# Performance work log

Hardware: AMD Instinct MI355X
Metric: run time of the kernel (lower is better)

## Reference

```python
import jax, jax.numpy as jnp
import numpy as np
import math

B = 2
D = 256
NH, NL, NP = 8, 4, 4
DH = D // NH
DFF = 1024
NLAYERS = 6
SHAPES = [(96, 96), (48, 48), (24, 24), (12, 12)]
CINS = [256, 512, 768, 1024]
LQ = sum(h * w for h, w in SHAPES)


def setup_inputs() -> dict:
    key = jax.random.key(0)
    ks = iter(jax.random.split(key, 64))
    inp = {}
    for i, (cin, (h, w)) in enumerate(zip(CINS, SHAPES)):
        inp[f"x{i+1}"] = jax.random.normal(next(ks), (B, cin, h, w), jnp.float32)
        inp[f"fc{i+1}_w"] = jax.random.normal(next(ks), (D, cin), jnp.float32) / np.sqrt(cin)
        inp[f"fc{i+1}_b"] = jnp.zeros((D,), jnp.float32)
    inp["gn_g"] = jnp.ones((4, D), jnp.float32)
    inp["gn_b"] = jnp.zeros((4, D), jnp.float32)
    inp["level_embed"] = jax.random.normal(next(ks), (4, D), jnp.float32)
    def lin(k, o, i_, s=1.0):
        return jax.random.normal(k, (NLAYERS, o, i_), jnp.float32) * (s / np.sqrt(i_))
    inp["off_w"] = lin(next(ks), NH * NL * NP * 2, D, 0.01)  # small, like zero-init offsets
    inp["off_b"] = jax.random.normal(next(ks), (NLAYERS, NH * NL * NP * 2), jnp.float32) * 0.5
    inp["aw_w"] = lin(next(ks), NH * NL * NP, D)
    inp["aw_b"] = jnp.zeros((NLAYERS, NH * NL * NP), jnp.float32)
    inp["val_w"] = lin(next(ks), D, D)
    inp["val_b"] = jnp.zeros((NLAYERS, D), jnp.float32)
    inp["out_w"] = lin(next(ks), D, D)
    inp["out_b"] = jnp.zeros((NLAYERS, D), jnp.float32)
    inp["ln1_g"] = jnp.ones((NLAYERS, D), jnp.float32)
    inp["ln1_b"] = jnp.zeros((NLAYERS, D), jnp.float32)
    inp["l1_w"] = lin(next(ks), DFF, D)
    inp["l1_b"] = jnp.zeros((NLAYERS, DFF), jnp.float32)
    inp["l2_w"] = lin(next(ks), D, DFF)
    inp["l2_b"] = jnp.zeros((NLAYERS, D), jnp.float32)
    inp["ln2_g"] = jnp.ones((NLAYERS, D), jnp.float32)
    inp["ln2_b"] = jnp.zeros((NLAYERS, D), jnp.float32)
    return inp


def layer_norm(x, g, b, eps=1e-5):
    m = x.mean(-1, keepdims=True)
    v = ((x - m) ** 2).mean(-1, keepdims=True)
    return (x - m) / jnp.sqrt(v + eps) * g + b


def group_norm(x, g, b, groups=32, eps=1e-5):
    # x: [B, L, C]; torch GroupNorm applied on [B, C, L] -> normalize over (group-channels, L)
    Bq, L, C = x.shape
    xg = x.reshape(Bq, L, groups, C // groups)
    m = xg.mean(axis=(1, 3), keepdims=True)
    v = ((xg - m) ** 2).mean(axis=(1, 3), keepdims=True)
    xg = (xg - m) / jnp.sqrt(v + eps)
    return xg.reshape(Bq, L, C) * g + b


def sine_pos(Hl, Wl):
    # DETR PositionEmbeddingSine, normalize=True, mask all-zero -> cumsum = arange(1..)
    eps, scale, T, npf = 1e-6, 2 * math.pi, 10000.0, D // 2
    ye = (jnp.arange(1, Hl + 1, dtype=jnp.float32) / (Hl + eps)) * scale
    xe = (jnp.arange(1, Wl + 1, dtype=jnp.float32) / (Wl + eps)) * scale
    dim_t = T ** (2 * (jnp.arange(npf) // 2).astype(jnp.float32) / npf)
    def emb(e):
        p = e[:, None] / dim_t
        return jnp.stack([jnp.sin(p[:, 0::2]), jnp.cos(p[:, 1::2])], -1).reshape(-1, npf)
    py, px = emb(ye), emb(xe)
    pos = jnp.concatenate([
        jnp.broadcast_to(py[:, None, :], (Hl, Wl, npf)),
        jnp.broadcast_to(px[None, :, :], (Hl, Wl, npf))], -1)
    return pos.reshape(Hl * Wl, D)


def ref_points():
    # training path: all levels, valid_ratios == 1 (masks all zero)
    refs = []
    for (Hl, Wl) in SHAPES:
        ry = (jnp.arange(Hl, dtype=jnp.float32) + 0.5) / Hl
        rx = (jnp.arange(Wl, dtype=jnp.float32) + 0.5) / Wl
        gy, gx = jnp.meshgrid(ry, rx, indexing='ij')
        refs.append(jnp.stack([gx.ravel(), gy.ravel()], -1))
    r = jnp.concatenate(refs, 0)  # [LQ, 2]
    return jnp.broadcast_to(r[None, :, None, :], (B, LQ, NL, 2))


def ms_deform(value, locs, attw):
    # value: [B, Lin, NH, DH]; locs: [B, Lq, NH, NL, NP, 2] in [0,1]; attw: [B, Lq, NH, NL, NP]
    Bq, Lq = locs.shape[0], locs.shape[1]
    out = jnp.zeros((Bq, Lq, NH, DH), value.dtype)
    start = 0
    for l, (Hl, Wl) in enumerate(SHAPES):
        vf = value[:, start:start + Hl * Wl].transpose(0, 2, 1, 3)  # [B, NH, HW, DH]
        start += Hl * Wl
        loc = locs[:, :, :, l]  # [B, Lq, NH, NP, 2]
        # grid_sample align_corners=False unnormalize: (2u-1+1)/2*W - 0.5 = u*W - 0.5
        x = loc[..., 0] * Wl - 0.5
        y = loc[..., 1] * Hl - 0.5
        x0, y0 = jnp.floor(x), jnp.floor(y)
        tx, ty = x - x0, y - y0
        samp = jnp.zeros((Bq, NH, Lq * NP, DH), value.dtype)
        for dx, dy, w in ((0, 0, (1 - tx) * (1 - ty)), (1, 0, tx * (1 - ty)),
                          (0, 1, (1 - tx) * ty), (1, 1, tx * ty)):
            xi, yi = x0 + dx, y0 + dy
            valid = (xi >= 0) & (xi < Wl) & (yi >= 0) & (yi < Hl)  # zero padding
            idx = (jnp.clip(yi, 0, Hl - 1) * Wl + jnp.clip(xi, 0, Wl - 1)).astype(jnp.int32)
            idxr = idx.transpose(0, 2, 1, 3).reshape(Bq, NH, Lq * NP)
            g = jnp.take_along_axis(vf, idxr[..., None], axis=2)  # [B, NH, Lq*NP, DH]
            wr = (w * valid).transpose(0, 2, 1, 3).reshape(Bq, NH, Lq * NP, 1)
            samp = samp + g * wr
        samp = samp.reshape(Bq, NH, Lq, NP, DH)
        out = out + jnp.einsum('bnqpd,bqnp->bqnd', samp, attw[:, :, :, l])
    return out.reshape(Bq, Lq, NH * DH)


def enc_layer(src, pos, ref, p):
    q = src + pos
    Bq, Lq, _ = src.shape
    off = (q @ p['off_w'].T + p['off_b']).reshape(Bq, Lq, NH, NL, NP, 2)
    aw = jax.nn.softmax((q @ p['aw_w'].T + p['aw_b']).reshape(Bq, Lq, NH, NL * NP), -1)
    aw = aw.reshape(Bq, Lq, NH, NL, NP)
    val = (src @ p['val_w'].T + p['val_b']).reshape(Bq, Lq, NH, DH)
    norml = jnp.array([[w, h] for (h, w) in SHAPES], jnp.float32)  # [NL, 2] as (W, H)
    locs = ref[:, :, None, :, None, :] + off / norml[None, None, None, :, None, :]
    att = ms_deform(val, locs, aw) @ p['out_w'].T + p['out_b']
    src = layer_norm(src + att, p['ln1_g'], p['ln1_b'])
    h = jax.nn.relu(src @ p['l1_w'].T + p['l1_b'])
    src = layer_norm(src + h @ p['l2_w'].T + p['l2_b'], p['ln2_g'], p['ln2_b'])
    return src


LAYER_KEYS = ['off_w', 'off_b', 'aw_w', 'aw_b', 'val_w', 'val_b', 'out_w', 'out_b',
              'ln1_g', 'ln1_b', 'l1_w', 'l1_b', 'l2_w', 'l2_b', 'ln2_g', 'ln2_b']


def _forward(x1, x2, x3, x4, fcs, gn_g, gn_b, level_embed, stacks):
    xs = [x1, x2, x3, x4]
    toks, poss = [], []
    for i, x in enumerate(xs):
        Bq, c, h, w = x.shape
        f = x.reshape(Bq, c, h * w).transpose(0, 2, 1)  # b (h w) c
        t = group_norm(f @ fcs[i][0].T + fcs[i][1], gn_g[i], gn_b[i])
        toks.append(t)
        poss.append(jnp.broadcast_to((sine_pos(h, w) + level_embed[i])[None], (Bq, h * w, D)))
    src = jnp.concatenate(toks, 1)
    pos = jnp.concatenate(poss, 1)
    ref = ref_points()
    for l in range(NLAYERS):
        p = {k: stacks[k][l] for k in LAYER_KEYS}
        src = enc_layer(src, pos, ref, p)
    return src


def reference(x1, x2, x3, x4, fc1_w, fc1_b, fc2_w, fc2_b, fc3_w, fc3_b, fc4_w, fc4_b,
              gn_g, gn_b, level_embed, off_w, off_b, aw_w, aw_b, val_w, val_b, out_w, out_b,
              ln1_g, ln1_b, l1_w, l1_b, l2_w, l2_b, ln2_g, ln2_b):
    fcs = [(fc1_w, fc1_b), (fc2_w, fc2_b), (fc3_w, fc3_b), (fc4_w, fc4_b)]
    stacks = dict(off_w=off_w, off_b=off_b, aw_w=aw_w, aw_b=aw_b, val_w=val_w, val_b=val_b,
                  out_w=out_w, out_b=out_b, ln1_g=ln1_g, ln1_b=ln1_b, l1_w=l1_w, l1_b=l1_b,
                  l2_w=l2_w, l2_b=l2_b, ln2_g=ln2_g, ln2_b=ln2_b)
    src = _forward(x1, x2, x3, x4, fcs, gn_g, gn_b, level_embed, stacks)
    spatial_shapes = jnp.array(SHAPES, jnp.int32)
    level_start_index = jnp.concatenate([jnp.zeros((1,), jnp.int32),
                                         jnp.cumsum(spatial_shapes.prod(1))[:-1]])
    valid_ratios = jnp.ones((B, NL, 2), jnp.float32)
    return (src, level_start_index, spatial_shapes, valid_ratios)
```

## Files before the change

kernel.cpp:

```cpp
#include <hip/hip_runtime.h>
#include <math.h>

#define DD 256
#define DFFN 1024
#define LQT 12240
#define BB 2
#define MROWS (BB * LQT)

typedef __attribute__((ext_vector_type(8))) short short8v;
typedef __attribute__((ext_vector_type(4))) float floatx4;

__device__ __forceinline__ unsigned short f2bf(float x) {
    unsigned int u = __builtin_bit_cast(unsigned int, x);
    u = (u + 0x7fffu + ((u >> 16) & 1u)) >> 16;
    return (unsigned short)u;
}
__device__ __forceinline__ float bf2f(unsigned short h) {
    unsigned int u = ((unsigned int)h) << 16;
    return __builtin_bit_cast(float, u);
}

__device__ __forceinline__ void gload16(const unsigned short* g, unsigned short* lds) {
    __builtin_amdgcn_global_load_lds(
        (const __attribute__((address_space(1))) unsigned int*)g,
        (__attribute__((address_space(3))) unsigned int*)lds, 16, 0, 0);
}

__device__ __forceinline__ void level_of(int q, int& lvl, int& start, int& S) {
    if (q < 9216)       { lvl = 0; start = 0;     S = 96; }
    else if (q < 11520) { lvl = 1; start = 9216;  S = 48; }
    else if (q < 12096) { lvl = 2; start = 11520; S = 24; }
    else                { lvl = 3; start = 12096; S = 12; }
}

__global__ __launch_bounds__(256)
void gemm_qkv(const unsigned short* __restrict__ Aq,
              const unsigned short* __restrict__ Asr,
              const unsigned short* __restrict__ Woff,
              const unsigned short* __restrict__ Waw,
              const unsigned short* __restrict__ Wval,
              const float* __restrict__ boff, const float* __restrict__ baw,
              const float* __restrict__ bval,
              float* __restrict__ awbo, unsigned short* __restrict__ offo,
              unsigned short* __restrict__ valo)
{
    __shared__ alignas(16) unsigned short As[2][4][64][8];
    __shared__ alignas(16) unsigned short Bs[2][4][128][8];
    const int t = threadIdx.x;
    const int m0 = blockIdx.x * 64;
    const int y = blockIdx.y;
    const unsigned short* A; const unsigned short* Wb; const float* bi;
    int nb, mode;
    if (y < 3) {
        A = Aq;
        if (y < 2) { Wb = Woff; bi = boff; nb = y * 128; mode = 0; }
        else       { Wb = Waw;  bi = baw;  nb = 0;       mode = 1; }
    } else {
        A = Asr; Wb = Wval; bi = bval; nb = (y - 3) * 128; mode = 2;
    }
    const int wv = __builtin_amdgcn_readfirstlane(t >> 6);
    const int lane = t & 63;
    const int wm = wv >> 1, wn = wv & 1;
    const int kb = lane >> 4, lr = lane & 15;

    const int ar = min(m0 + lane, MROWS - 1);
    const unsigned short* gA  = A  + (long)ar * 256 + wv * 8;
    const unsigned short* gB0 = Wb + (long)(nb + lane) * 256 + wv * 8;
    const unsigned short* gB1 = Wb + (long)(nb + 64 + lane) * 256 + wv * 8;

    floatx4 acc[2][4];
    #pragma unroll
    for (int m = 0; m < 2; ++m)
        #pragma unroll
        for (int n = 0; n < 4; ++n)
            acc[m][n] = (floatx4){0.f, 0.f, 0.f, 0.f};

    gload16(gA,  &As[0][wv][0][0]);
    gload16(gB0, &Bs[0][wv][0][0]);
    gload16(gB1, &Bs[0][wv][64][0]);
    gA += 32; gB0 += 32; gB1 += 32;
    __syncthreads();

    #pragma unroll
    for (int kt = 0; kt < 8; ++kt) {
        const int cur = kt & 1;
        if (kt < 7) {
            gload16(gA,  &As[cur ^ 1][wv][0][0]);
            gload16(gB0, &Bs[cur ^ 1][wv][0][0]);
            gload16(gB1, &Bs[cur ^ 1][wv][64][0]);
            gA += 32; gB0 += 32; gB1 += 32;
        }
        short8v av[2], bv[4];
        #pragma unroll
        for (int m = 0; m < 2; ++m)
            av[m] = *(const short8v*)&As[cur][kb][wm * 32 + m * 16 + lr][0];
        #pragma unroll
        for (int n = 0; n < 4; ++n)
            bv[n] = *(const short8v*)&Bs[cur][kb][wn * 64 + n * 16 + lr][0];
        #pragma unroll
        for (int m = 0; m < 2; ++m)
            #pragma unroll
            for (int n = 0; n < 4; ++n)
                acc[m][n] = __builtin_amdgcn_mfma_f32_16x16x32_bf16(
                    av[m], bv[n], acc[m][n], 0, 0, 0);
        __syncthreads();
    }

    const int lh = lane >> 4;
    #pragma unroll
    for (int m = 0; m < 2; ++m) {
        const int row0 = m0 + wm * 32 + m * 16 + lh * 4;
        #pragma unroll
        for (int n = 0; n < 4; ++n) {
            const int col = nb + wn * 64 + n * 16 + lr;
            const float b = bi[col];
            #pragma unroll
            for (int r = 0; r < 4; ++r) {
                const int row = row0 + r;
                if (row >= MROWS) continue;
                const float v = acc[m][n][r] + b;
                if (mode == 0)      offo[(long)row * 256 + col] = f2bf(v);
                else if (mode == 1) awbo[(long)row * 128 + col] = v;
                else                valo[(long)row * 256 + col] = f2bf(v);
            }
        }
    }
}

__global__ __launch_bounds__(256)
void gemm64(const unsigned short* __restrict__ A, long aZ,
            const unsigned short* __restrict__ W,
            const float* __restrict__ bias,
            float* __restrict__ Cf, long cZ,
            int M, int N, int K)
{
    __shared__ alignas(16) unsigned short As[2][4][64][8];
    __shared__ alignas(16) unsigned short Bs[2][4][128][8];
    const int t = threadIdx.x;
    const int z = blockIdx.z;
    A  += (long)z * aZ;
    Cf += (long)z * cZ;
    const int m0 = blockIdx.x * 64;
    const int n0 = blockIdx.y * 128;
    const int wv = __builtin_amdgcn_readfirstlane(t >> 6);
    const int lane = t & 63;
    const int wm = wv >> 1, wn = wv & 1;
    const int kb = lane >> 4, lr = lane & 15;

    const int ar = min(m0 + lane, M - 1);
    const unsigned short* gA  = A + (long)ar * K + wv * 8;
    const unsigned short* gB0 = W + (long)(n0 + lane) * K + wv * 8;
    const unsigned short* gB1 = W + (long)(n0 + 64 + lane) * K + wv * 8;

    floatx4 acc[2][4];
    #pragma unroll
    for (int m = 0; m < 2; ++m)
        #pragma unroll
        for (int n = 0; n < 4; ++n)
            acc[m][n] = (floatx4){0.f, 0.f, 0.f, 0.f};

    gload16(gA,  &As[0][wv][0][0]);
    gload16(gB0, &Bs[0][wv][0][0]);
    gload16(gB1, &Bs[0][wv][64][0]);
    gA += 32; gB0 += 32; gB1 += 32;
    __syncthreads();

    const int nk = K >> 5;
    for (int kt = 0; kt < nk; ++kt) {
        const int cur = kt & 1;
        if (kt + 1 < nk) {
            gload16(gA,  &As[cur ^ 1][wv][0][0]);
            gload16(gB0, &Bs[cur ^ 1][wv][0][0]);
            gload16(gB1, &Bs[cur ^ 1][wv][64][0]);
            gA += 32; gB0 += 32; gB1 += 32;
        }
        short8v av[2], bv[4];
        #pragma unroll
        for (int m = 0; m < 2; ++m)
            av[m] = *(const short8v*)&As[cur][kb][wm * 32 + m * 16 + lr][0];
        #pragma unroll
        for (int n = 0; n < 4; ++n)
            bv[n] = *(const short8v*)&Bs[cur][kb][wn * 64 + n * 16 + lr][0];
        #pragma unroll
        for (int m = 0; m < 2; ++m)
            #pragma unroll
            for (int n = 0; n < 4; ++n)
                acc[m][n] = __builtin_amdgcn_mfma_f32_16x16x32_bf16(
                    av[m], bv[n], acc[m][n], 0, 0, 0);
        __syncthreads();
    }

    const int lh = lane >> 4;
    #pragma unroll
    for (int m = 0; m < 2; ++m) {
        const int row0 = m0 + wm * 32 + m * 16 + lh * 4;
        #pragma unroll
        for (int n = 0; n < 4; ++n) {
            const int col = n0 + wn * 64 + n * 16 + lr;
            const float b = bias[col];
            #pragma unroll
            for (int r = 0; r < 4; ++r) {
                const int row = row0 + r;
                if (row >= M) continue;
                Cf[(long)row * N + col] = acc[m][n][r] + b;
            }
        }
    }
}

__global__ __launch_bounds__(256)
void gemm128(const unsigned short* __restrict__ A,
             const unsigned short* __restrict__ W,
             const float* __restrict__ bias, unsigned short* __restrict__ Ch,
             int M, int N, int K)
{
    __shared__ alignas(16) unsigned short As[2][4][128][8];
    __shared__ alignas(16) unsigned short Bs[2][4][128][8];
    const int t = threadIdx.x;
    const int m0 = blockIdx.x * 128;
    const int n0 = blockIdx.y * 128;
    const int wv = __builtin_amdgcn_readfirstlane(t >> 6);
    const int lane = t & 63;
    const int wm = wv >> 1, wn = wv & 1;
    const int kb = lane >> 4, lr = lane & 15;

    const int r0 = min(m0 + lane, M - 1);
    const int r1 = min(m0 + 64 + lane, M - 1);
    const unsigned short* gA0 = A + (long)r0 * K + wv * 8;
    const unsigned short* gA1 = A + (long)r1 * K + wv * 8;
    const unsigned short* gB0 = W + (long)(n0 + lane) * K + wv * 8;
    const unsigned short* gB1 = W + (long)(n0 + 64 + lane) * K + wv * 8;

    floatx4 acc[4][4];
    #pragma unroll
    for (int m = 0; m < 4; ++m)
        #pragma unroll
        for (int n = 0; n < 4; ++n)
            acc[m][n] = (floatx4){0.f, 0.f, 0.f, 0.f};

    gload16(gA0, &As[0][wv][0][0]);
    gload16(gA1, &As[0][wv][64][0]);
    gload16(gB0, &Bs[0][wv][0][0]);
    gload16(gB1, &Bs[0][wv][64][0]);
    gA0 += 32; gA1 += 32; gB0 += 32; gB1 += 32;
    __syncthreads();

    const int nk = K >> 5;
    for (int kt = 0; kt < nk; ++kt) {
        const int cur = kt & 1;
        if (kt + 1 < nk) {
            gload16(gA0, &As[cur ^ 1][wv][0][0]);
            gload16(gA1, &As[cur ^ 1][wv][64][0]);
            gload16(gB0, &Bs[cur ^ 1][wv][0][0]);
            gload16(gB1, &Bs[cur ^ 1][wv][64][0]);
            gA0 += 32; gA1 += 32; gB0 += 32; gB1 += 32;
        }
        short8v av[4], bv[4];
        #pragma unroll
        for (int m = 0; m < 4; ++m)
            av[m] = *(const short8v*)&As[cur][kb][wm * 64 + m * 16 + lr][0];
        #pragma unroll
        for (int n = 0; n < 4; ++n)
            bv[n] = *(const short8v*)&Bs[cur][kb][wn * 64 + n * 16 + lr][0];
        #pragma unroll
        for (int m = 0; m < 4; ++m)
            #pragma unroll
            for (int n = 0; n < 4; ++n)
                acc[m][n] = __builtin_amdgcn_mfma_f32_16x16x32_bf16(
                    av[m], bv[n], acc[m][n], 0, 0, 0);
        __syncthreads();
    }

    const int lh = lane >> 4;
    #pragma unroll
    for (int m = 0; m < 4; ++m) {
        const int row0 = m0 + wm * 64 + m * 16 + lh * 4;
        #pragma unroll
        for (int n = 0; n < 4; ++n) {
            const int col = n0 + wn * 64 + n * 16 + lr;
            const float b = bias[col];
            #pragma unroll
            for (int r = 0; r < 4; ++r) {
                const int row = row0 + r;
                if (row >= M) continue;
                Ch[(long)row * N + col] = f2bf(fmaxf(acc[m][n][r] + b, 0.f));
            }
        }
    }
}

__global__ __launch_bounds__(256)
void gemm_ln(const unsigned short* __restrict__ A,
             const unsigned short* __restrict__ W,
             const float* __restrict__ bias, const unsigned short* R,
             const float* __restrict__ lg, const float* __restrict__ lb,
             float* outf, unsigned short* outh,
             const float* __restrict__ pos, unsigned short* __restrict__ qout,
             int M, int K)
{
    __shared__ alignas(16) unsigned short As[2][4][32][8];
    __shared__ alignas(16) unsigned short Bs[2][4][256][8];
    __shared__ float red[32][4][2];
    __shared__ float smean[32], sinv[32];
    const int t = threadIdx.x;
    const int m0 = blockIdx.x * 32;
    const int wv = __builtin_amdgcn_readfirstlane(t >> 6);
    const int lane = t & 63;
    const int kb = lane >> 4, lr = lane & 15;
    const int lh = kb;

    const unsigned short* gA = A + (long)(m0 + (lane & 31)) * K
                                 + (wv * 2 + (lane >> 5)) * 8;
    const unsigned short* gB0 = W + (long)lane * K + wv * 8;
    const unsigned short* gB1 = W + (long)(64 + lane) * K + wv * 8;
    const unsigned short* gB2 = W + (long)(128 + lane) * K + wv * 8;
    const unsigned short* gB3 = W + (long)(192 + lane) * K + wv * 8;

    floatx4 acc[2][4];
    #pragma unroll
    for (int m = 0; m < 2; ++m)
        #pragma unroll
        for (int n = 0; n < 4; ++n)
            acc[m][n] = (floatx4){0.f, 0.f, 0.f, 0.f};

    if (wv < 2) gload16(gA, &As[0][wv * 2][0][0]);
    gload16(gB0, &Bs[0][wv][0][0]);
    gload16(gB1, &Bs[0][wv][64][0]);
    gload16(gB2, &Bs[0][wv][128][0]);
    gload16(gB3, &Bs[0][wv][192][0]);
    gA += 32; gB0 += 32; gB1 += 32; gB2 += 32; gB3 += 32;
    __syncthreads();

    const int nk = K >> 5;
    for (int kt = 0; kt < nk; ++kt) {
        const int cur = kt & 1;
        if (kt + 1 < nk) {
            if (wv < 2) gload16(gA, &As[cur ^ 1][wv * 2][0][0]);
            gload16(gB0, &Bs[cur ^ 1][wv][0][0]);
            gload16(gB1, &Bs[cur ^ 1][wv][64][0]);
            gload16(gB2, &Bs[cur ^ 1][wv][128][0]);
            gload16(gB3, &Bs[cur ^ 1][wv][192][0]);
            gA += 32; gB0 += 32; gB1 += 32; gB2 += 32; gB3 += 32;
        }
        short8v av[2], bv[4];
        #pragma unroll
        for (int m = 0; m < 2; ++m)
            av[m] = *(const short8v*)&As[cur][kb][m * 16 + lr][0];
        #pragma unroll
        for (int n = 0; n < 4; ++n)
            bv[n] = *(const short8v*)&Bs[cur][kb][wv * 64 + n * 16 + lr][0];
        #pragma unroll
        for (int m = 0; m < 2; ++m)
            #pragma unroll
            for (int n = 0; n < 4; ++n)
                acc[m][n] = __builtin_amdgcn_mfma_f32_16x16x32_bf16(
                    av[m], bv[n], acc[m][n], 0, 0, 0);
        __syncthreads();
    }

    #pragma unroll
    for (int n = 0; n < 4; ++n) {
        const int col = wv * 64 + n * 16 + lr;
        const float bcol = bias[col];
        #pragma unroll
        for (int m = 0; m < 2; ++m) {
            #pragma unroll
            for (int r = 0; r < 4; ++r) {
                const int grow = m0 + m * 16 + lh * 4 + r;
                acc[m][n][r] += bcol + bf2f(R[(long)grow * 256 + col]);
            }
        }
    }
    #pragma unroll
    for (int m = 0; m < 2; ++m) {
        #pragma unroll
        for (int r = 0; r < 4; ++r) {
            float s = acc[m][0][r] + acc[m][1][r] + acc[m][2][r] + acc[m][3][r];
            float q = acc[m][0][r] * acc[m][0][r] + acc[m][1][r] * acc[m][1][r]
                    + acc[m][2][r] * acc[m][2][r] + acc[m][3][r] * acc[m][3][r];
            #pragma unroll
            for (int o = 1; o < 16; o <<= 1) {
                s += __shfl_xor(s, o);
                q += __shfl_xor(q, o);
            }
            if (lr == 0) {
                red[m * 16 + lh * 4 + r][wv][0] = s;
                red[m * 16 + lh * 4 + r][wv][1] = q;
            }
        }
    }
    __syncthreads();
    if (t < 32) {
        const float s = red[t][0][0] + red[t][1][0] + red[t][2][0] + red[t][3][0];
        const float q = red[t][0][1] + red[t][1][1] + red[t][2][1] + red[t][3][1];
        const float mean = s * (1.f / 256.f);
        smean[t] = mean;
        sinv[t] = rsqrtf(q * (1.f / 256.f) - mean * mean + 1e-5f);
    }
    __syncthreads();
    #pragma unroll
    for (int n = 0; n < 4; ++n) {
        const int col = wv * 64 + n * 16 + lr;
        const float gc = lg[col], bc = lb[col];
        #pragma unroll
        for (int m = 0; m < 2; ++m) {
            #pragma unroll
            for (int r = 0; r < 4; ++r) {
                const int row = m * 16 + lh * 4 + r;
                const int grow = m0 + row;
                const float y = (acc[m][n][r] - smean[row]) * sinv[row] * gc + bc;
                const long o = (long)grow * 256 + col;
                outh[o] = f2bf(y);
                if (outf) outf[o] = y;
                if (qout) {
                    const int qrow = grow - (grow >= LQT ? LQT : 0);
                    qout[o] = f2bf(y + pos[(long)qrow * 256 + col]);
                }
            }
        }
    }
}

__global__ __launch_bounds__(256)
void tp_k(const float* __restrict__ x, unsigned short* __restrict__ xt,
          int C, int Ml)
{
    __shared__ float tile[32][33];
    const int m0 = blockIdx.x * 32, c0 = blockIdx.y * 32;
    const int zb = blockIdx.z;
    const float* px = x + (long)zb * C * Ml;
    unsigned short* pxt = xt + (long)zb * Ml * C;
    const int t = threadIdx.x;
    {
        const int cl = t >> 3, m4 = (t & 7) * 4;
        const int gm = m0 + m4;
        if (gm < Ml) {
            const float4 v = *(const float4*)(px + (long)(c0 + cl) * Ml + gm);
            tile[cl][m4 + 0] = v.x; tile[cl][m4 + 1] = v.y;
            tile[cl][m4 + 2] = v.z; tile[cl][m4 + 3] = v.w;
        }
    }
    __syncthreads();
    {
        const int ml = t >> 3, c4 = (t & 7) * 4;
        const int gm = m0 + ml;
        if (gm < Ml) {
            ushort4 o;
            o.x = f2bf(tile[c4 + 0][ml]);
            o.y = f2bf(tile[c4 + 1][ml]);
            o.z = f2bf(tile[c4 + 2][ml]);
            o.w = f2bf(tile[c4 + 3][ml]);
            *(ushort4*)(pxt + (long)gm * C + c0 + c4) = o;
        }
    }
}

__global__ __launch_bounds__(256)
void gn_part(const float* __restrict__ src, float* __restrict__ part)
{
    const int x = blockIdx.x;
    const int b = x >> 7, c = x & 127;
    int lvl, chunk;
    if (c < 96)       { lvl = 0; chunk = c; }
    else if (c < 120) { lvl = 1; chunk = c - 96; }
    else if (c < 126) { lvl = 2; chunk = c - 120; }
    else              { lvl = 3; chunk = c - 126; }
    const int starts[4] = {0, 9216, 11520, 12096};
    const int crows[4]  = {96, 96, 96, 72};
    const int rows = crows[lvl];
    const long base = ((long)b * LQT + starts[lvl] + (long)chunk * rows) * DD;
    const int t = threadIdx.x;
    float s = 0.f, sq = 0.f;
    for (int r = 0; r < rows; ++r) {
        const float v = src[base + (long)r * DD + t];
        s += v; sq += v * v;
    }
    #pragma unroll
    for (int o = 1; o < 8; o <<= 1) {
        s  += __shfl_xor(s, o);
        sq += __shfl_xor(sq, o);
    }
    if ((t & 7) == 0) {
        float* p = part + ((long)x * 32 + (t >> 3)) * 2;
        p[0] = s; p[1] = sq;
    }
}

__global__ void gn_fin(const float* __restrict__ part, float* __restrict__ stat)
{
    const int t = threadIdx.x;
    const int b = t >> 7, rest = t & 127;
    const int lvl = rest >> 5, grp = rest & 31;
    const int cbase[4] = {0, 96, 120, 126};
    const int ccnt[4]  = {96, 24, 6, 2};
    const int Ml[4]    = {9216, 2304, 576, 144};
    float s = 0.f, sq = 0.f;
    for (int i = 0; i < ccnt[lvl]; ++i) {
        const float* p = part + ((long)(b * 128 + cbase[lvl] + i) * 32 + grp) * 2;
        s += p[0]; sq += p[1];
    }
    const float cnt = (float)(Ml[lvl] * 8);
    const float mean = s / cnt;
    const float inv = rsqrtf(sq / cnt - mean * mean + 1e-5f);
    float* o = stat + ((b * 4 + lvl) * 32 + grp) * 2;
    o[0] = mean; o[1] = inv;
}

__global__ __launch_bounds__(256)
void gn_apply(const float* __restrict__ src, unsigned short* __restrict__ srch,
              unsigned short* __restrict__ qout,
              const float* __restrict__ stat,
              const float* __restrict__ gg, const float* __restrict__ gb,
              const float* __restrict__ pos)
{
    const int t = threadIdx.x;
    const long row = (long)blockIdx.x * 4 + (t >> 6);
    const int lane = t & 63;
    const int b = row >= LQT;
    const int q = (int)row - b * LQT;
    int lvl, start, S;
    level_of(q, lvl, start, S);
    const float2 ms = *(const float2*)(stat + ((b * 4 + lvl) * 32 + (lane >> 1)) * 2);
    const int col = lane * 4;
    const float4 v  = *(const float4*)(src + row * DD + col);
    const float4 gv = *(const float4*)(gg + lvl * DD + col);
    const float4 bv = *(const float4*)(gb + lvl * DD + col);
    float4 y;
    y.x = (v.x - ms.x) * ms.y * gv.x + bv.x;
    y.y = (v.y - ms.x) * ms.y * gv.y + bv.y;
    y.z = (v.z - ms.x) * ms.y * gv.z + bv.z;
    y.w = (v.w - ms.x) * ms.y * gv.w + bv.w;
    ushort4 hh;
    hh.x = f2bf(y.x); hh.y = f2bf(y.y); hh.z = f2bf(y.z); hh.w = f2bf(y.w);
    *(ushort4*)(srch + row * DD + col) = hh;
    const float4 pv = *(const float4*)(pos + (long)q * DD + col);
    ushort4 qq;
    qq.x = f2bf(y.x + pv.x); qq.y = f2bf(y.y + pv.y);
    qq.z = f2bf(y.z + pv.z); qq.w = f2bf(y.w + pv.w);
    *(ushort4*)(qout + row * DD + col) = qq;
}

__global__ __launch_bounds__(256)
void pos_k(float* __restrict__ pos, const float* __restrict__ lemb)
{
    const int q = blockIdx.x;
    const int d = threadIdx.x;
    int lvl, start, S;
    level_of(q, lvl, start, S);
    const int qi = q - start;
    const int r = qi / S, c = qi % S;
    const float twopi = 6.283185307179586f;
    float e; int dd;
    if (d < 128) { e = (float)(r + 1) / ((float)S + 1e-6f) * twopi; dd = d; }
    else         { e = (float)(c + 1) / ((float)S + 1e-6f) * twopi; dd = d - 128; }
    const float dimt = expf(9.210340371976184f * (float)(dd & ~1) / 128.f);
    const float p = e / dimt;
    const float v = (dd & 1) ? cosf(p) : sinf(p);
    pos[(long)q * DD + d] = v + lemb[lvl * DD + d];
}

__global__ __launch_bounds__(256)
void msdeform_k(const unsigned short* __restrict__ val,
                const unsigned short* __restrict__ off,
                const float* __restrict__ aw,
                unsigned short* __restrict__ out)
{
    __shared__ int   s_base[2][128][5];
    __shared__ float s_w[2][128][5];
    const int t = threadIdx.x;
    const int j = t >> 7;
    const int tt = t & 127;
    const int bid = blockIdx.x;
    const int sb = (bid & 7) * 1530 + (bid >> 3);
    const int bq = sb * 2 + j;
    const int b = bq >= LQT;
    const int q = bq - b * LQT;
    int lvl0, start0, S0;
    level_of(q, lvl0, start0, S0);
    const int qi = q - start0;
    {
        const int lv = (tt >> 2) & 3;
        const int SL[4]  = {96, 48, 24, 12};
        const int STL[4] = {0, 9216, 11520, 12096};
        const int S = SL[lv];
        const float refx = ((float)(qi % S0) + 0.5f) / (float)S0;
        const float refy = ((float)(qi / S0) + 0.5f) / (float)S0;
        const unsigned int ou = *(const unsigned int*)(off + (long)bq * 256 + 2 * tt);
        const float x = refx * (float)S - 0.5f + bf2f((unsigned short)(ou & 0xffffu));
        const float y = refy * (float)S - 0.5f + bf2f((unsigned short)(ou >> 16));
        const float logit = aw[(long)bq * 128 + tt];
        float mx = logit;
        #pragma unroll
        for (int s_ = 1; s_ < 16; s_ <<= 1) mx = fmaxf(mx, __shfl_xor(mx, s_));
        const float e = __expf(logit - mx);
        float sum = e;
        #pragma unroll
        for (int s_ = 1; s_ < 16; s_ <<= 1) sum += __shfl_xor(sum, s_);
        const float wat = e / sum;
        const float x0 = floorf(x), y0 = floorf(y);
        const float tx = x - x0, ty = y - y0;
        const int ix = (int)x0, iy = (int)y0;
        #pragma unroll
        for (int c = 0; c < 4; ++c) {
            const int dx = c & 1, dy = c >> 1;
            const int xi = ix + dx, yi = iy + dy;
            const bool ok = (xi >= 0) && (xi < S) && (yi >= 0) && (yi < S);
            const int cx = min(max(xi, 0), S - 1);
            const int cy = min(max(yi, 0), S - 1);
            const float wxy = (dx ? tx : 1.f - tx) * (dy ? ty : 1.f - ty);
            s_base[j][tt][c] = (STL[lv] + cy * S + cx) * 256;
            s_w[j][tt][c] = ok ? wxy * wat : 0.f;
        }
    }
    __syncthreads();
    const int h = tt >> 4, d8 = (tt >> 2) & 3, sub = tt & 3;
    const unsigned short* vb = val + (long)b * (LQT * DD) + h * 32 + d8 * 8;
    float a0 = 0.f, a1 = 0.f, a2 = 0.f, a3 = 0.f;
    float a4 = 0.f, a5 = 0.f, a6 = 0.f, a7 = 0.f;
    #pragma unroll
    for (int i = 0; i < 4; ++i) {
        const int task = h * 16 + i * 4 + sub;
        #pragma unroll
        for (int c = 0; c < 4; ++c) {
            const float wv = s_w[j][task][c];
            const uint4 g = *(const uint4*)(vb + s_base[j][task][c]);
            a0 = fmaf(wv, bf2f((unsigned short)(g.x & 0xffffu)), a0);
            a1 = fmaf(wv, bf2f((unsigned short)(g.x >> 16)), a1);
            a2 = fmaf(wv, bf2f((unsigned short)(g.y & 0xffffu)), a2);
            a3 = fmaf(wv, bf2f((unsigned short)(g.y >> 16)), a3);
            a4 = fmaf(wv, bf2f((unsigned short)(g.z & 0xffffu)), a4);
            a5 = fmaf(wv, bf2f((unsigned short)(g.z >> 16)), a5);
            a6 = fmaf(wv, bf2f((unsigned short)(g.w & 0xffffu)), a6);
            a7 = fmaf(wv, bf2f((unsigned short)(g.w >> 16)), a7);
        }
    }
    #pragma unroll
    for (int o = 1; o < 4; o <<= 1) {
        a0 += __shfl_xor(a0, o); a1 += __shfl_xor(a1, o);
        a2 += __shfl_xor(a2, o); a3 += __shfl_xor(a3, o);
        a4 += __shfl_xor(a4, o); a5 += __shfl_xor(a5, o);
        a6 += __shfl_xor(a6, o); a7 += __shfl_xor(a7, o);
    }
    if (sub == 0) {
        uint4 o;
        o.x = (unsigned)f2bf(a0) | ((unsigned)f2bf(a1) << 16);
        o.y = (unsigned)f2bf(a2) | ((unsigned)f2bf(a3) << 16);
        o.z = (unsigned)f2bf(a4) | ((unsigned)f2bf(a5) << 16);
        o.w = (unsigned)f2bf(a6) | ((unsigned)f2bf(a7) << 16);
        *(uint4*)(out + (long)bq * DD + h * 32 + d8 * 8) = o;
    }
}

#define WCVT_TOTAL 5177344L
__global__ __launch_bounds__(256)
void wcvt_k(const float* __restrict__ s0, const float* __restrict__ s1,
            const float* __restrict__ s2, const float* __restrict__ s3,
            const float* __restrict__ s4, const float* __restrict__ s5,
            const float* __restrict__ s6, const float* __restrict__ s7,
            const float* __restrict__ s8, const float* __restrict__ s9,
            unsigned short* __restrict__ dst)
{
    const long i = ((long)blockIdx.x * 256 + threadIdx.x) * 4;
    if (i >= WCVT_TOTAL) return;
    const float* sp; long base;
    if (i < 1048576) {
        if (i < 655360) {
            if (i < 65536)       { sp = s0; base = 0; }
            else if (i < 196608) { sp = s1; base = 65536; }
            else if (i < 393216) { sp = s2; base = 196608; }
            else                 { sp = s3; base = 393216; }
        } else                   { sp = s4; base = 655360; }
    } else if (i < 2031616) {
        if (i < 1245184)         { sp = s5; base = 1048576; }
        else if (i < 1638400)    { sp = s6; base = 1245184; }
        else                     { sp = s7; base = 1638400; }
    } else if (i < 3604480)      { sp = s8; base = 2031616; }
    else                         { sp = s9; base = 3604480; }
    const float4 v = *(const float4*)(sp + (i - base));
    ushort4 o;
    o.x = f2bf(v.x); o.y = f2bf(v.y); o.z = f2bf(v.z); o.w = f2bf(v.w);
    *(ushort4*)(dst + i) = o;
}

__global__ void tail_k(float* __restrict__ o)
{
    const float tv[28] = {0.f, 9216.f, 11520.f, 12096.f,
                          96.f, 96.f, 48.f, 48.f, 24.f, 24.f, 12.f, 12.f,
                          1.f, 1.f, 1.f, 1.f, 1.f, 1.f, 1.f, 1.f,
                          1.f, 1.f, 1.f, 1.f, 1.f, 1.f, 1.f, 1.f};
    const int t = threadIdx.x;
    if (t < 28) o[t] = tv[t];
}

extern "C" void kernel_launch(void* const* d_in, const int* in_sizes, int n_in,
                              void* d_out, int out_size, void* d_ws, size_t ws_size,
                              hipStream_t stream)
{
    const float* xs[4]  = {(const float*)d_in[0], (const float*)d_in[3],
                           (const float*)d_in[6], (const float*)d_in[9]};
    const float* fcw[4] = {(const float*)d_in[1], (const float*)d_in[4],
                           (const float*)d_in[7], (const float*)d_in[10]};
    const float* fcb[4] = {(const float*)d_in[2], (const float*)d_in[5],
                           (const float*)d_in[8], (const float*)d_in[11]};
    const float* gn_g = (const float*)d_in[12];
    const float* gn_b = (const float*)d_in[13];
    const float* lemb = (const float*)d_in[14];
    const float* off_w = (const float*)d_in[15];
    const float* off_b = (const float*)d_in[16];
    const float* aw_w  = (const float*)d_in[17];
    const float* aw_b  = (const float*)d_in[18];
    const float* val_w = (const float*)d_in[19];
    const float* val_b = (const float*)d_in[20];
    const float* out_w = (const float*)d_in[21];
    const float* out_b = (const float*)d_in[22];
    const float* ln1_g = (const float*)d_in[23];
    const float* ln1_b = (const float*)d_in[24];
    const float* l1_w  = (const float*)d_in[25];
    const float* l1_b  = (const float*)d_in[26];
    const float* l2_w  = (const float*)d_in[27];
    const float* l2_b  = (const float*)d_in[28];
    const float* ln2_g = (const float*)d_in[29];
    const float* ln2_b = (const float*)d_in[30];

    float* src = (float*)d_out;
    float* ws = (float*)d_ws;
    float* pos = ws;
    float* awb = pos + 3133440;
    unsigned short* bigbuf = (unsigned short*)(awb + 3133440);
    unsigned short* xt     = bigbuf;
    unsigned short* off_bf = bigbuf;
    unsigned short* val_bf = bigbuf + 6266880;
    unsigned short* msd_bf = bigbuf + 12533760;
    unsigned short* hid_bf = bigbuf;
    unsigned short* q_bf   = bigbuf + 25067520;
    unsigned short* src_bf = q_bf + 6266880;
    unsigned short* wb     = src_bf + 6266880;
    unsigned short* wb_fc[4];
    wb_fc[0] = wb;
    wb_fc[1] = wb_fc[0] + 65536;
    wb_fc[2] = wb_fc[1] + 131072;
    wb_fc[3] = wb_fc[2] + 196608;
    unsigned short* wb_off = wb_fc[3] + 262144;
    unsigned short* wb_aw  = wb_off + 393216;
    unsigned short* wb_val = wb_aw  + 196608;
    unsigned short* wb_out = wb_val + 393216;
    unsigned short* wb_l1  = wb_out + 393216;
    unsigned short* wb_l2  = wb_l1  + 1572864;
    float* part = (float*)(wb_l2 + 1572864);
    float* stat = part + 16384;
    (void)in_sizes; (void)n_in; (void)out_size; (void)ws_size;

    const int CINS[4]   = {256, 512, 768, 1024};
    const int SS[4]     = {96, 48, 24, 12};
    const int STARTS[4] = {0, 9216, 11520, 12096};
    const long XTOFF[4] = {0, 4718592, 7077888, 7962624};

    pos_k<<<LQT, 256, 0, stream>>>(pos, lemb);
    wcvt_k<<<(WCVT_TOTAL / 4 + 255) / 256, 256, 0, stream>>>(
        fcw[0], fcw[1], fcw[2], fcw[3], off_w, aw_w, val_w, out_w, l1_w, l2_w, wb);

    for (int i = 0; i < 4; ++i) {
        const int Ml = SS[i] * SS[i];
        tp_k<<<dim3((Ml + 31) / 32, CINS[i] / 32, BB), 256, 0, stream>>>(
            xs[i], xt + XTOFF[i], CINS[i], Ml);
    }
    for (int i = 0; i < 4; ++i) {
        const int Ml = SS[i] * SS[i];
        gemm64<<<dim3((Ml + 63) / 64, 2, BB), 256, 0, stream>>>(
            xt + XTOFF[i], (long)Ml * CINS[i],
            wb_fc[i], fcb[i],
            src + (long)STARTS[i] * DD, (long)LQT * DD,
            Ml, DD, CINS[i]);
    }
    gn_part<<<256, 256, 0, stream>>>(src, part);
    gn_fin<<<1, 256, 0, stream>>>(part, stat);
    gn_apply<<<MROWS / 4, 256, 0, stream>>>(src, src_bf, q_bf, stat, gn_g, gn_b, pos);

    for (int l = 0; l < 6; ++l) {
        gemm_qkv<<<dim3(383, 5), 256, 0, stream>>>(
            q_bf, src_bf,
            wb_off + (long)l * 65536, wb_aw + (long)l * 32768,
            wb_val + (long)l * 65536,
            off_b + l * DD, aw_b + l * 128, val_b + l * DD,
            awb, off_bf, val_bf);
        msdeform_k<<<MROWS / 2, 256, 0, stream>>>(val_bf, off_bf, awb, msd_bf);
        gemm_ln<<<765, 256, 0, stream>>>(
            msd_bf, wb_out + (long)l * 65536, out_b + l * DD, src_bf,
            ln1_g + l * DD, ln1_b + l * DD, nullptr, src_bf,
            nullptr, nullptr, MROWS, DD);
        gemm128<<<dim3(192, 8), 256, 0, stream>>>(
            src_bf, wb_l1 + (long)l * 262144, l1_b + l * DFFN, hid_bf,
            MROWS, DFFN, DD);
        const bool last = (l == 5);
        gemm_ln<<<765, 256, 0, stream>>>(
            hid_bf, wb_l2 + (long)l * 262144, l2_b + l * DD, src_bf,
            ln2_g + l * DD, ln2_b + l * DD, last ? src : nullptr, src_bf,
            last ? nullptr : pos, last ? nullptr : q_bf, MROWS, DFFN);
    }
    tail_k<<<1, 32, 0, stream>>>(src + (long)BB * LQT * DD);
}
```

Before: 1.593 ms.

## Fuse FFN linear1+ReLU+linear2+LayerNorm into one kernel keeping hidden in LDS

Replaces the separate gemm128 (linear1+ReLU writing a 24480x1024 bf16 hidden buffer) and the second gemm_ln with a single fused_ffn kernel. Each 32-row block computes its 1024-wide hidden activation in LDS, then runs the second GEMM, residual add and LayerNorm directly from it. This removes the global write and reread of the hidden tensor. The cost is ~113KB of dynamic LDS per block (low occupancy), 32-row tiles that reload all FFN weights per block, and a switch of the positional add to a bf16 copy of pos. gemm_ln is also specialised to K=256 with a fully unrolled loop.

```diff
diff --git a/kernel.cpp b/kernel.cpp
--- a/kernel.cpp
+++ b/kernel.cpp
@@ -209,94 +209,11 @@
 }
 
 __global__ __launch_bounds__(256)
-void gemm128(const unsigned short* __restrict__ A,
-             const unsigned short* __restrict__ W,
-             const float* __restrict__ bias, unsigned short* __restrict__ Ch,
-             int M, int N, int K)
-{
-    __shared__ alignas(16) unsigned short As[2][4][128][8];
-    __shared__ alignas(16) unsigned short Bs[2][4][128][8];
-    const int t = threadIdx.x;
-    const int m0 = blockIdx.x * 128;
-    const int n0 = blockIdx.y * 128;
-    const int wv = __builtin_amdgcn_readfirstlane(t >> 6);
-    const int lane = t & 63;
-    const int wm = wv >> 1, wn = wv & 1;
-    const int kb = lane >> 4, lr = lane & 15;
-
-    const int r0 = min(m0 + lane, M - 1);
-    const int r1 = min(m0 + 64 + lane, M - 1);
-    const unsigned short* gA0 = A + (long)r0 * K + wv * 8;
-    const unsigned short* gA1 = A + (long)r1 * K + wv * 8;
-    const unsigned short* gB0 = W + (long)(n0 + lane) * K + wv * 8;
-    const unsigned short* gB1 = W + (long)(n0 + 64 + lane) * K + wv * 8;
-
-    floatx4 acc[4][4];
-    #pragma unroll
-    for (int m = 0; m < 4; ++m)
-        #pragma unroll
-        for (int n = 0; n < 4; ++n)
-            acc[m][n] = (floatx4){0.f, 0.f, 0.f, 0.f};
-
-    gload16(gA0, &As[0][wv][0][0]);
-    gload16(gA1, &As[0][wv][64][0]);
-    gload16(gB0, &Bs[0][wv][0][0]);
-    gload16(gB1, &Bs[0][wv][64][0]);
-    gA0 += 32; gA1 += 32; gB0 += 32; gB1 += 32;
-    __syncthreads();
-
-    const int nk = K >> 5;
-    for (int kt = 0; kt < nk; ++kt) {
-        const int cur = kt & 1;
-        if (kt + 1 < nk) {
-            gload16(gA0, &As[cur ^ 1][wv][0][0]);
-            gload16(gA1, &As[cur ^ 1][wv][64][0]);
-            gload16(gB0, &Bs[cur ^ 1][wv][0][0]);
-            gload16(gB1, &Bs[cur ^ 1][wv][64][0]);
-            gA0 += 32; gA1 += 32; gB0 += 32; gB1 += 32;
-        }
-        short8v av[4], bv[4];
-        #pragma unroll
-        for (int m = 0; m < 4; ++m)
-            av[m] = *(const short8v*)&As[cur][kb][wm * 64 + m * 16 + lr][0];
-        #pragma unroll
-        for (int n = 0; n < 4; ++n)
-            bv[n] = *(const short8v*)&Bs[cur][kb][wn * 64 + n * 16 + lr][0];
-        #pragma unroll
-        for (int m = 0; m < 4; ++m)
-            #pragma unroll
-            for (int n = 0; n < 4; ++n)
-                acc[m][n] = __builtin_amdgcn_mfma_f32_16x16x32_bf16(
-                    av[m], bv[n], acc[m][n], 0, 0, 0);
-        __syncthreads();
-    }
-
-    const int lh = lane >> 4;
-    #pragma unroll
-    for (int m = 0; m < 4; ++m) {
-        const int row0 = m0 + wm * 64 + m * 16 + lh * 4;
-        #pragma unroll
-        for (int n = 0; n < 4; ++n) {
-            const int col = n0 + wn * 64 + n * 16 + lr;
-            const float b = bias[col];
-            #pragma unroll
-            for (int r = 0; r < 4; ++r) {
-                const int row = row0 + r;
-                if (row >= M) continue;
-                Ch[(long)row * N + col] = f2bf(fmaxf(acc[m][n][r] + b, 0.f));
-            }
-        }
-    }
-}
-
-__global__ __launch_bounds__(256)
 void gemm_ln(const unsigned short* __restrict__ A,
              const unsigned short* __restrict__ W,
              const float* __restrict__ bias, const unsigned short* R,
              const float* __restrict__ lg, const float* __restrict__ lb,
-             float* outf, unsigned short* outh,
-             const float* __restrict__ pos, unsigned short* __restrict__ qout,
-             int M, int K)
+             unsigned short* outh, int M)
 {
     __shared__ alignas(16) unsigned short As[2][4][32][8];
     __shared__ alignas(16) unsigned short Bs[2][4][256][8];
@@ -309,12 +226,12 @@
     const int kb = lane >> 4, lr = lane & 15;
     const int lh = kb;
 
-    const unsigned short* gA = A + (long)(m0 + (lane & 31)) * K
+    const unsigned short* gA = A + (long)(m0 + (lane & 31)) * 256
                                  + (wv * 2 + (lane >> 5)) * 8;
-    const unsigned short* gB0 = W + (long)lane * K + wv * 8;
-    const unsigned short* gB1 = W + (long)(64 + lane) * K + wv * 8;
-    const unsigned short* gB2 = W + (long)(128 + lane) * K + wv * 8;
-    const unsigned short* gB3 = W + (long)(192 + lane) * K + wv * 8;
+    const unsigned short* gB0 = W + (long)lane * 256 + wv * 8;
+    const unsigned short* gB1 = W + (long)(64 + lane) * 256 + wv * 8;
+    const unsigned short* gB2 = W + (long)(128 + lane) * 256 + wv * 8;
+    const unsigned short* gB3 = W + (long)(192 + lane) * 256 + wv * 8;
 
     floatx4 acc[2][4];
     #pragma unroll
@@ -331,10 +248,10 @@
     gA += 32; gB0 += 32; gB1 += 32; gB2 += 32; gB3 += 32;
     __syncthreads();
 
-    const int nk = K >> 5;
-    for (int kt = 0; kt < nk; ++kt) {
+    #pragma unroll
+    for (int kt = 0; kt < 8; ++kt) {
         const int cur = kt & 1;
-        if (kt + 1 < nk) {
+        if (kt < 7) {
             if (wv < 2) gload16(gA, &As[cur ^ 1][wv * 2][0][0]);
             gload16(gB0, &Bs[cur ^ 1][wv][0][0]);
             gload16(gB1, &Bs[cur ^ 1][wv][64][0]);
@@ -407,14 +324,203 @@
             #pragma unroll
             for (int r = 0; r < 4; ++r) {
                 const int row = m * 16 + lh * 4 + r;
+                const float y = (acc[m][n][r] - smean[row]) * sinv[row] * gc + bc;
+                outh[(long)(m0 + row) * 256 + col] = f2bf(y);
+            }
+        }
+    }
+}
+
+__global__ __launch_bounds__(256)
+void fused_ffn(const unsigned short* __restrict__ A,
+               const unsigned short* __restrict__ W1,
+               const float* __restrict__ b1,
+               const unsigned short* __restrict__ W2,
+               const float* __restrict__ b2,
+               const unsigned short* R,
+               const float* __restrict__ lg, const float* __restrict__ lb,
+               float* outf, unsigned short* outh,
+               const unsigned short* __restrict__ pos_bf,
+               unsigned short* __restrict__ qout)
+{
+    extern __shared__ __align__(16) unsigned short lds[];
+    unsigned short* A_s = lds;
+    unsigned short* hid = lds + 8192;
+    unsigned short* Ws  = lds + 40960;
+    float* red   = (float*)(lds + 57344);
+    float* smean = red + 256;
+    float* sinv  = smean + 32;
+
+    const int t = threadIdx.x;
+    const int m0 = blockIdx.x * 32;
+    const int wv = __builtin_amdgcn_readfirstlane(t >> 6);
+    const int lane = t & 63;
+    const int kb = lane >> 4, lr = lane & 15;
+    const int lh = kb;
+
+    #pragma unroll
+    for (int i = 0; i < 4; ++i) {
+        const int c = wv * 4 + i;
+        gload16(A + (long)(m0 + (lane & 31)) * 256 + (c * 2 + (lane >> 5)) * 8,
+                A_s + c * 512);
+    }
+    {
+        const unsigned short* src = W1 + (long)(lane) * 256 + wv * 8;
+        gload16(src,                 Ws + ((0 * 4 + wv) * 256 + 0) * 8);
+        gload16(src + (long)64*256,  Ws + ((0 * 4 + wv) * 256 + 64) * 8);
+    }
+    __syncthreads();
+
+    floatx4 acc1[2][2];
+    #pragma unroll
+    for (int m = 0; m < 2; ++m)
+        #pragma unroll
+        for (int n = 0; n < 2; ++n)
+            acc1[m][n] = (floatx4){0.f, 0.f, 0.f, 0.f};
+
+    for (int tt = 0; tt < 64; ++tt) {
+        const int cur = tt & 1;
+        if (tt + 1 < 64) {
+            const int nc1 = (tt + 1) >> 3, ks1 = (tt + 1) & 7;
+            const unsigned short* src = W1 + (long)(nc1 * 128 + lane) * 256
+                                           + ks1 * 32 + wv * 8;
+            unsigned short* dst = Ws + (((cur ^ 1) * 4 + wv) * 256) * 8;
+            gload16(src,                dst);
+            gload16(src + (long)64*256, dst + 64 * 8);
+        }
+        const int ks = tt & 7;
+        short8v av[2], bv[2];
+        #pragma unroll
+        for (int m = 0; m < 2; ++m)
+            av[m] = *(const short8v*)&A_s[((ks * 4 + kb) * 32 + m * 16 + lr) * 8];
+        #pragma unroll
+        for (int n = 0; n < 2; ++n)
+            bv[n] = *(const short8v*)&Ws[((cur * 4 + kb) * 256 + wv * 32 + n * 16 + lr) * 8];
+        #pragma unroll
+        for (int m = 0; m < 2; ++m)
+            #pragma unroll
+            for (int n = 0; n < 2; ++n)
+                acc1[m][n] = __builtin_amdgcn_mfma_f32_16x16x32_bf16(
+                    av[m], bv[n], acc1[m][n], 0, 0, 0);
+        if (ks == 7) {
+            const int nc = tt >> 3;
+            #pragma unroll
+            for (int n = 0; n < 2; ++n) {
+                const int col = nc * 128 + wv * 32 + n * 16 + lr;
+                const float bc = b1[col];
+                #pragma unroll
+                for (int m = 0; m < 2; ++m) {
+                    #pragma unroll
+                    for (int r = 0; r < 4; ++r) {
+                        const int row = m * 16 + lh * 4 + r;
+                        const float v = fmaxf(acc1[m][n][r] + bc, 0.f);
+                        hid[((col >> 3) * 32 + row) * 8 + (col & 7)] = f2bf(v);
+                    }
+                    acc1[m][n] = (floatx4){0.f, 0.f, 0.f, 0.f};
+                }
+            }
+        }
+        __syncthreads();
+    }
+
+    {
+        const unsigned short* src = W2 + (long)lane * 1024 + wv * 8;
+        unsigned short* dst = Ws + ((0 * 4 + wv) * 256) * 8;
+        #pragma unroll
+        for (int i = 0; i < 4; ++i)
+            gload16(src + (long)i * 64 * 1024, dst + i * 64 * 8);
+    }
+    __syncthreads();
+
+    floatx4 acc2[2][4];
+    #pragma unroll
+    for (int m = 0; m < 2; ++m)
+        #pragma unroll
+        for (int n = 0; n < 4; ++n)
+            acc2[m][n] = (floatx4){0.f, 0.f, 0.f, 0.f};
+
+    for (int h = 0; h < 32; ++h) {
+        const int cur = h & 1;
+        if (h + 1 < 32) {
+            const unsigned short* src = W2 + (long)lane * 1024 + (h + 1) * 32 + wv * 8;
+            unsigned short* dst = Ws + (((cur ^ 1) * 4 + wv) * 256) * 8;
+            #pragma unroll
+            for (int i = 0; i < 4; ++i)
+                gload16(src + (long)i * 64 * 1024, dst + i * 64 * 8);
+        }
+        short8v av[2], bv[4];
+        #pragma unroll
+        for (int m = 0; m < 2; ++m)
+            av[m] = *(const short8v*)&hid[((h * 4 + kb) * 32 + m * 16 + lr) * 8];
+        #pragma unroll
+        for (int n = 0; n < 4; ++n)
+            bv[n] = *(const short8v*)&Ws[((cur * 4 + kb) * 256 + wv * 64 + n * 16 + lr) * 8];
+        #pragma unroll
+        for (int m = 0; m < 2; ++m)
+            #pragma unroll
+            for (int n = 0; n < 4; ++n)
+                acc2[m][n] = __builtin_amdgcn_mfma_f32_16x16x32_bf16(
+                    av[m], bv[n], acc2[m][n], 0, 0, 0);
+        __syncthreads();
+    }
+
+    #pragma unroll
+    for (int n = 0; n < 4; ++n) {
+        const int col = wv * 64 + n * 16 + lr;
+        const float bcol = b2[col];
+        #pragma unroll
+        for (int m = 0; m < 2; ++m) {
+            #pragma unroll
+            for (int r = 0; r < 4; ++r) {
+                const int grow = m0 + m * 16 + lh * 4 + r;
+                acc2[m][n][r] += bcol + bf2f(R[(long)grow * 256 + col]);
+            }
+        }
+    }
+    #pragma unroll
+    for (int m = 0; m < 2; ++m) {
+        #pragma unroll
+        for (int r = 0; r < 4; ++r) {
+            float s = acc2[m][0][r] + acc2[m][1][r] + acc2[m][2][r] + acc2[m][3][r];
+            float q = acc2[m][0][r] * acc2[m][0][r] + acc2[m][1][r] * acc2[m][1][r]
+                    + acc2[m][2][r] * acc2[m][2][r] + acc2[m][3][r] * acc2[m][3][r];
+            #pragma unroll
+            for (int o = 1; o < 16; o <<= 1) {
+                s += __shfl_xor(s, o);
+                q += __shfl_xor(q, o);
+            }
+            if (lr == 0) {
+                red[(m * 16 + lh * 4 + r) * 8 + wv * 2 + 0] = s;
+                red[(m * 16 + lh * 4 + r) * 8 + wv * 2 + 1] = q;
+            }
+        }
+    }
+    __syncthreads();
+    if (t < 32) {
+        const float s = red[t*8+0] + red[t*8+2] + red[t*8+4] + red[t*8+6];
+        const float q = red[t*8+1] + red[t*8+3] + red[t*8+5] + red[t*8+7];
+        const float mean = s * (1.f / 256.f);
+        smean[t] = mean;
+        sinv[t] = rsqrtf(q * (1.f / 256.f) - mean * mean + 1e-5f);
+    }
+    __syncthreads();
+    #pragma unroll
+    for (int n = 0; n < 4; ++n) {
+        const int col = wv * 64 + n * 16 + lr;
+        const float gc = lg[col], bc = lb[col];
+        #pragma unroll
+        for (int m = 0; m < 2; ++m) {
+            #pragma unroll
+            for (int r = 0; r < 4; ++r) {
+                const int row = m * 16 + lh * 4 + r;
                 const int grow = m0 + row;
-                const float y = (acc[m][n][r] - smean[row]) * sinv[row] * gc + bc;
+                const float y = (acc2[m][n][r] - smean[row]) * sinv[row] * gc + bc;
                 const long o = (long)grow * 256 + col;
                 outh[o] = f2bf(y);
                 if (outf) outf[o] = y;
                 if (qout) {
                     const int qrow = grow - (grow >= LQT ? LQT : 0);
-                    qout[o] = f2bf(y + pos[(long)qrow * 256 + col]);
+                    qout[o] = f2bf(y + bf2f(pos_bf[(long)qrow * 256 + col]));
                 }
             }
         }
@@ -541,7 +647,8 @@
 }
 
 __global__ __launch_bounds__(256)
-void pos_k(float* __restrict__ pos, const float* __restrict__ lemb)
+void pos_k(float* __restrict__ pos, unsigned short* __restrict__ pos_bf,
+           const float* __restrict__ lemb)
 {
     const int q = blockIdx.x;
     const int d = threadIdx.x;
@@ -555,8 +662,9 @@
     else         { e = (float)(c + 1) / ((float)S + 1e-6f) * twopi; dd = d - 128; }
     const float dimt = expf(9.210340371976184f * (float)(dd & ~1) / 128.f);
     const float p = e / dimt;
-    const float v = (dd & 1) ? cosf(p) : sinf(p);
-    pos[(long)q * DD + d] = v + lemb[lvl * DD + d];
+    const float v = ((dd & 1) ? cosf(p) : sinf(p)) + lemb[lvl * DD + d];
+    pos[(long)q * DD + d] = v;
+    pos_bf[(long)q * DD + d] = f2bf(v);
 }
 
 __global__ __launch_bounds__(256)
@@ -731,7 +839,6 @@
     unsigned short* off_bf = bigbuf;
     unsigned short* val_bf = bigbuf + 6266880;
     unsigned short* msd_bf = bigbuf + 12533760;
-    unsigned short* hid_bf = bigbuf;
     unsigned short* q_bf   = bigbuf + 25067520;
     unsigned short* src_bf = q_bf + 6266880;
     unsigned short* wb     = src_bf + 6266880;
@@ -748,6 +855,7 @@
     unsigned short* wb_l2  = wb_l1  + 1572864;
     float* part = (float*)(wb_l2 + 1572864);
     float* stat = part + 16384;
+    unsigned short* pos_bf = (unsigned short*)(stat + 512);
     (void)in_sizes; (void)n_in; (void)out_size; (void)ws_size;
 
     const int CINS[4]   = {256, 512, 768, 1024};
@@ -755,7 +863,7 @@
     const int STARTS[4] = {0, 9216, 11520, 12096};
     const long XTOFF[4] = {0, 4718592, 7077888, 7962624};
 
-    pos_k<<<LQT, 256, 0, stream>>>(pos, lemb);
+    pos_k<<<LQT, 256, 0, stream>>>(pos, pos_bf, lemb);
     wcvt_k<<<(WCVT_TOTAL / 4 + 255) / 256, 256, 0, stream>>>(
         fcw[0], fcw[1], fcw[2], fcw[3], off_w, aw_w, val_w, out_w, l1_w, l2_w, wb);
 
@@ -786,16 +894,14 @@
         msdeform_k<<<MROWS / 2, 256, 0, stream>>>(val_bf, off_bf, awb, msd_bf);
         gemm_ln<<<765, 256, 0, stream>>>(
             msd_bf, wb_out + (long)l * 65536, out_b + l * DD, src_bf,
-            ln1_g + l * DD, ln1_b + l * DD, nullptr, src_bf,
-            nullptr, nullptr, MROWS, DD);
-        gemm128<<<dim3(192, 8), 256, 0, stream>>>(
-            src_bf, wb_l1 + (long)l * 262144, l1_b + l * DFFN, hid_bf,
-            MROWS, DFFN, DD);
+            ln1_g + l * DD, ln1_b + l * DD, src_bf, MROWS);
         const bool last = (l == 5);
-        gemm_ln<<<765, 256, 0, stream>>>(
-            hid_bf, wb_l2 + (long)l * 262144, l2_b + l * DD, src_bf,
-            ln2_g + l * DD, ln2_b + l * DD, last ? src : nullptr, src_bf,
-            last ? nullptr : pos, last ? nullptr : q_bf, MROWS, DFFN);
+        fused_ffn<<<765, 256, 115968, stream>>>(
+            src_bf, wb_l1 + (long)l * 262144, l1_b + l * DFFN,
+            wb_l2 + (long)l * 262144, l2_b + l * DD,
+            src_bf, ln2_g + l * DD, ln2_b + l * DD,
+            last ? src : nullptr, src_bf,
+            pos_bf, last ? nullptr : q_bf);
     }
     tail_k<<<1, 32, 0, stream>>>(src + (long)BB * LQT * DD);
 }
```

Result: slower. 1.939 ms (+21.7%).
